# Performance work log

Measured on AMD Instinct MI355X. Metric: run time of the kernel, lower is better.

## Reference

```python
import jax, jax.numpy as jnp
import numpy as np

N_HEADS = 16
N_KV_HEADS = 4
HEAD_DIM = 128
D_MODEL = 2048
WINDOW = 1024
THETA = 10000.0
EPS = 1e-6


def _rmsnorm(x, w):
    var = jnp.mean(x * x, axis=-1, keepdims=True)
    return x * jax.lax.rsqrt(var + EPS) * w


def _rope(x, pos):
    # x: [B, H, S, D]; rotate-half (llama-style) RoPE
    d2 = HEAD_DIM // 2
    inv_freq = 1.0 / (THETA ** (jnp.arange(0, HEAD_DIM, 2, dtype=jnp.float32) / HEAD_DIM))
    ang = pos[:, None].astype(jnp.float32) * inv_freq[None, :]  # [S, D/2]
    cos = jnp.cos(ang)[None, None]
    sin = jnp.sin(ang)[None, None]
    x1, x2 = x[..., :d2], x[..., d2:]
    return jnp.concatenate([x1 * cos - x2 * sin, x1 * sin + x2 * cos], axis=-1)


def setup_inputs() -> dict:
    key = jax.random.key(0)
    ks = jax.random.split(key, 7)
    B, S = 1, 2048
    s = 0.02
    return {
        "x": jax.random.normal(ks[0], (B, S, D_MODEL), jnp.float32),
        "wq": jax.random.normal(ks[1], (N_HEADS * HEAD_DIM, D_MODEL), jnp.float32) * s,
        "wk": jax.random.normal(ks[2], (N_KV_HEADS * HEAD_DIM, D_MODEL), jnp.float32) * s,
        "wv": jax.random.normal(ks[3], (N_KV_HEADS * HEAD_DIM, D_MODEL), jnp.float32) * s,
        "wo": jax.random.normal(ks[4], (D_MODEL, N_HEADS * HEAD_DIM), jnp.float32) * s,
        "q_norm_w": jnp.ones((HEAD_DIM,), jnp.float32),
        "k_norm_w": jnp.ones((HEAD_DIM,), jnp.float32),
    }


def reference(x, wq, wk, wv, wo, q_norm_w, k_norm_w):
    B, S, _ = x.shape
    past_length = 0
    scale = HEAD_DIM ** -0.5
    n_rep = N_HEADS // N_KV_HEADS

    q = (x @ wq.T).reshape(B, S, N_HEADS, HEAD_DIM).transpose(0, 2, 1, 3)
    k = (x @ wk.T).reshape(B, S, N_KV_HEADS, HEAD_DIM).transpose(0, 2, 1, 3)
    v = (x @ wv.T).reshape(B, S, N_KV_HEADS, HEAD_DIM).transpose(0, 2, 1, 3)

    q = _rmsnorm(q, q_norm_w)
    k = _rmsnorm(k, k_norm_w)

    pos = jnp.arange(S) + past_length
    q = _rope(q, pos)
    k = _rope(k, pos)

    # GQA: materialize repeated KV heads, as in _repeat_kv
    k_rep = jnp.repeat(k, n_rep, axis=1)  # [B, H, S, D]
    v_rep = jnp.repeat(v, n_rep, axis=1)

    # sliding-window causal mask (total_seq_len=S > WINDOW)
    q_idx = jnp.arange(S)[:, None] + past_length
    k_idx = jnp.arange(S)[None, :]
    mask = (q_idx >= k_idx) & (q_idx - k_idx < WINDOW)  # [S, S]

    scores = jnp.einsum("bhqd,bhkd->bhqk", q, k_rep) * scale
    scores = jnp.where(mask[None, None], scores, jnp.float32(-jnp.inf))
    attn = jax.nn.softmax(scores, axis=-1)
    out = jnp.einsum("bhqk,bhkd->bhqd", attn, v_rep)

    out = out.transpose(0, 2, 1, 3).reshape(B, S, N_HEADS * HEAD_DIM)
    return out @ wo.T
```

## Files before the change

kernel.cpp:

```cpp
#include <hip/hip_runtime.h>
#include <hip/hip_bf16.h>
#include <cstdint>
#include <cstddef>

typedef __attribute__((ext_vector_type(4))) float f32x4;
typedef __attribute__((ext_vector_type(8))) short bf16x8;
typedef __attribute__((ext_vector_type(8))) unsigned short us8;

#define MFMA16(a, b, c) __builtin_amdgcn_mfma_f32_16x16x32_bf16(a, b, c, 0, 0, 0)

__device__ inline unsigned short f2bf(float f) {
    unsigned int u = __float_as_uint(f);
    u += 0x7fffu + ((u >> 16) & 1u);
    return (unsigned short)(u >> 16);
}
__device__ inline unsigned short f2bf_fast(float f) {
    float r;
    asm("v_cvt_pk_bf16_f32 %0, %1, %2" : "=v"(r) : "v"(f), "v"(f));
    return (unsigned short)__float_as_uint(r);
}

__device__ inline void gload_lds16(const void* g, void* l) {
    __builtin_amdgcn_global_load_lds(
        (const __attribute__((address_space(1))) void*)g,
        (__attribute__((address_space(3))) void*)l, 16, 0, 0);
}
__device__ inline unsigned lds_addr(const void* p) {
    return (unsigned)(size_t)((__attribute__((address_space(3))) const void*)p);
}

__global__ __launch_bounds__(256) void prep_all(const float* __restrict__ x,
                                                const float* __restrict__ wq,
                                                const float* __restrict__ wk,
                                                const float* __restrict__ wv,
                                                const float* __restrict__ wo,
                                                unsigned short* __restrict__ xb,
                                                unsigned short* __restrict__ wqkv,
                                                unsigned short* __restrict__ wob,
                                                float2* __restrict__ tbl) {
    const int b = blockIdx.x;
    if (b < 14336) {
        const float* src; unsigned short* dst; int off4;
        if (b < 4096)       { src = x;  dst = xb;                 off4 = b; }
        else if (b < 8192)  { src = wq; dst = wqkv;               off4 = b - 4096; }
        else if (b < 9216)  { src = wk; dst = wqkv + 2048 * 2048; off4 = b - 8192; }
        else if (b < 10240) { src = wv; dst = wqkv + 2560 * 2048; off4 = b - 9216; }
        else                { src = wo; dst = wob;                off4 = b - 10240; }
        int i = (off4 * 256 + threadIdx.x) * 4;
        float4 v = *(const float4*)(src + i);
        ushort4 o;
        o.x = f2bf(v.x); o.y = f2bf(v.y); o.z = f2bf(v.z); o.w = f2bf(v.w);
        *(ushort4*)(dst + i) = o;
    } else {
        int idx = (b - 14336) * 256 + threadIdx.x;
        int row = idx >> 6, t = idx & 63;
        float inv_freq = exp2f((float)t * (-2.0f / 128.0f) * 13.287712379549449f);
        float s, c;
        sincosf((float)row * inv_freq, &s, &c);
        tbl[idx] = make_float2(c, s);
    }
}

__global__ __launch_bounds__(512, 2) void gemm256(const unsigned short* __restrict__ A,
                                                  const unsigned short* __restrict__ B,
                                                  float* __restrict__ Cp,
                                                  int M, int N, int Kfull, int kspan) {
    __shared__ unsigned short As[3][8192];
    __shared__ unsigned short Bs[3][8192];
    const int tid = threadIdx.x;
    const int lane = tid & 63, wave = tid >> 6;
    const int wr = wave >> 2, wc = wave & 3;
    const int l15 = lane & 15, l4 = lane >> 4;
    const int gx = gridDim.x;
    const int nwg = gx * gridDim.y;
    const int bid0 = blockIdx.y * gx + blockIdx.x;
    const int q8 = nwg >> 3, r8 = nwg & 7;
    const int xcd = bid0 & 7, sub = bid0 >> 3;
    const int wgid = ((xcd < r8) ? xcd * (q8 + 1) : r8 * (q8 + 1) + (xcd - r8) * q8) + sub;
    const int bm = wgid / gx, bn = wgid % gx;
    const int z = blockIdx.z;
    const unsigned short* Az = A + (size_t)z * kspan;
    const unsigned short* Bz = B + (size_t)z * kspan;
    float* C = Cp + (size_t)z * M * N;
    const int nK = kspan >> 5;

    f32x4 acc[8][4] = {};

    const int r0 = tid >> 2, qs = tid & 3;
    const int qsw = qs ^ ((r0 >> 1) & 3);
    const unsigned short* pa0 = Az + (size_t)(bm * 256 + r0) * Kfull + qsw * 8;
    const unsigned short* pa1 = pa0 + (size_t)128 * Kfull;
    const unsigned short* pb0 = Bz + (size_t)(bn * 256 + r0) * Kfull + qsw * 8;
    const unsigned short* pb1 = pb0 + (size_t)128 * Kfull;

#define STG(kt, bb)                                            \
    do {                                                       \
        gload_lds16(pa0 + (kt) * 32, &As[bb][tid * 8]);        \
        gload_lds16(pa1 + (kt) * 32, &As[bb][4096 + tid * 8]); \
        gload_lds16(pb0 + (kt) * 32, &Bs[bb][tid * 8]);        \
        gload_lds16(pb1 + (kt) * 32, &Bs[bb][4096 + tid * 8]); \
    } while (0)

    const int q = l4 ^ ((l15 >> 1) & 3);
    const unsigned aB = lds_addr(&As[0][0]) + (unsigned)((wr * 128 + l15) * 64 + q * 16);
    const unsigned bB = lds_addr(&Bs[0][0]) + (unsigned)((wc * 64 + l15) * 64 + q * 16);

#define DSR(dst, addr, off) \
    asm volatile("ds_read_b128 %0, %1 offset:" #off : "=v"(dst) : "v"(addr))

    STG(0, 0);
    STG(1, 1);
    int bc = 0, bs = 2;
    for (int kt = 0; kt < nK; ++kt) {
        if (kt + 1 < nK)
            asm volatile("s_waitcnt vmcnt(4)\ns_barrier" ::: "memory");
        else
            asm volatile("s_waitcnt vmcnt(0)\ns_barrier" ::: "memory");
        __builtin_amdgcn_sched_barrier(0);

        bf16x8 a[8], b[4];
        {
            const unsigned aA = aB + bc * 16384;
            const unsigned bA = bB + bc * 16384;
            DSR(a[0], aA, 0);    DSR(a[1], aA, 1024);
            DSR(a[2], aA, 2048); DSR(a[3], aA, 3072);
            DSR(a[4], aA, 4096); DSR(a[5], aA, 5120);
            DSR(a[6], aA, 6144); DSR(a[7], aA, 7168);
            DSR(b[0], bA, 0);    DSR(b[1], bA, 1024);
            DSR(b[2], bA, 2048); DSR(b[3], bA, 3072);
        }
        if (kt + 2 < nK) STG(kt + 2, bs);
        asm volatile("s_waitcnt lgkmcnt(0)" ::: "memory");
        __builtin_amdgcn_sched_barrier(0);

        __builtin_amdgcn_s_setprio(1);
#pragma unroll
        for (int m = 0; m < 8; ++m)
#pragma unroll
            for (int n = 0; n < 4; ++n)
                acc[m][n] = MFMA16(a[m], b[n], acc[m][n]);
        __builtin_amdgcn_s_setprio(0);

        if (++bc == 3) bc = 0;
        if (++bs == 3) bs = 0;
    }
#undef STG
#undef DSR

    for (int m = 0; m < 8; ++m)
        for (int n = 0; n < 4; ++n)
            for (int j = 0; j < 4; ++j) {
                int row = bm * 256 + wr * 128 + m * 16 + l4 * 4 + j;
                int col = bn * 256 + wc * 64 + n * 16 + l15;
                C[(size_t)row * N + col] = acc[m][n][j];
            }
}

__global__ __launch_bounds__(256) void norm_rope(const float* __restrict__ p0,
                                                 const float* __restrict__ p1,
                                                 const float* __restrict__ qw,
                                                 const float* __restrict__ kw,
                                                 const float2* __restrict__ tbl,
                                                 unsigned short* __restrict__ Qb,
                                                 unsigned short* __restrict__ Kb) {
    const int row = blockIdx.x;
    const int head = blockIdx.y * 4 + (threadIdx.x >> 6);
    const int t = threadIdx.x & 63;
    const size_t off = (size_t)row * 3072 + head * 128;
    float x1 = p0[off + t] + p1[off + t];
    float x2 = p0[off + t + 64] + p1[off + t + 64];
    float ss = x1 * x1 + x2 * x2;
    for (int m = 32; m; m >>= 1) ss += __shfl_xor(ss, m);
    float r = rsqrtf(ss * (1.0f / 128.0f) + 1e-6f);
    const float* w = (head < 16) ? qw : kw;
    float y1 = x1 * r * w[t], y2 = x2 * r * w[t + 64];
    float2 cs = tbl[row * 64 + t];
    x1 = y1 * cs.x - y2 * cs.y;
    x2 = y1 * cs.y + y2 * cs.x;
    if (head < 16) {
        const float SCALE2 = 0.12751879526654698f;
        x1 *= SCALE2; x2 *= SCALE2;
    }
    unsigned short* dst = (head < 16) ? Qb + ((size_t)head * 2048 + row) * 128
                                      : Kb + ((size_t)(head - 16) * 2048 + row) * 128;
    dst[t] = f2bf(x1);
    dst[t + 64] = f2bf(x2);
}

__global__ __launch_bounds__(256) void transpose_v(const float* __restrict__ p0,
                                                   const float* __restrict__ p1,
                                                   unsigned short* __restrict__ VbT) {
    const int kt = blockIdx.x;
    const int h  = blockIdx.y;
    __shared__ unsigned short T[64 * 132];
    const int tid = threadIdx.x;
    for (int i = 0; i < 8; ++i) {
        int s = i * 256 + tid;
        int r = s >> 5, c = (s & 31) * 4;
        size_t off = (size_t)(kt * 64 + r) * 3072 + (20 + h) * 128 + c;
        float4 a = *(const float4*)(p0 + off);
        float4 b = *(const float4*)(p1 + off);
        ushort4 o;
        o.x = f2bf(a.x + b.x); o.y = f2bf(a.y + b.y);
        o.z = f2bf(a.z + b.z); o.w = f2bf(a.w + b.w);
        *(ushort4*)&T[r * 132 + c] = o;
    }
    __syncthreads();
    for (int i = 0; i < 4; ++i) {
        int s = i * 256 + tid;
        int d = s >> 3, ck = (s & 7) * 8;
        us8 v;
        for (int j = 0; j < 8; ++j) v[j] = T[(ck + j) * 132 + d];
        *(us8*)(VbT + (size_t)h * 128 * 2048 + (size_t)d * 2048 + kt * 64 + ck) = v;
    }
}

__global__ __launch_bounds__(256) void attn_fwd(const unsigned short* __restrict__ Qb,
                                                const unsigned short* __restrict__ Kb,
                                                const unsigned short* __restrict__ VbT,
                                                unsigned short* __restrict__ Ob) {
    const int bid = blockIdx.x;
    const int seq = bid >> 3;
    const int h = (bid & 7) * 2 + (seq >> 5);
    const int qt = seq & 31;
    const int kvh = h >> 2;
    const int q0 = qt * 64;
    __shared__ unsigned short Ks[2][64 * 128];
    __shared__ unsigned short Vs[2][128 * 64];
    __shared__ unsigned short Ps[4][16 * 72];
    const int tid = threadIdx.x;
    const int lane = tid & 63, wave = tid >> 6;
    const int l15 = lane & 15, l4 = lane >> 4;

    bf16x8 qf[4];
    {
        const unsigned short* qrow =
            Qb + ((size_t)h * 2048 + q0 + wave * 16 + l15) * 128 + l4 * 8;
        for (int kk = 0; kk < 4; ++kk) qf[kk] = *(const bf16x8*)(qrow + kk * 32);
    }
    f32x4 o[8] = {};
    float m2[4], lp[4];
    for (int j = 0; j < 4; ++j) { m2[j] = -1e30f; lp[j] = 0.0f; }
    const int kt_lo = (qt >= 16) ? (qt - 16) : 0;

    const unsigned short* Kh = Kb + (size_t)kvh * 2048 * 128;
    const unsigned short* Vh = VbT + (size_t)kvh * 128 * 2048;

    {
        const int kt = kt_lo;
        for (int i = 0; i < 4; ++i) {
            int s = i * 256 + tid;
            int r = s >> 4;
            int cb = ((s & 15) * 16) ^ ((r & 7) << 4);
            gload_lds16(Kh + (size_t)(kt * 64 + r) * 128 + (cb >> 1), &Ks[0][s * 8]);
        }
        for (int i = 0; i < 4; ++i) {
            int s = i * 256 + tid;
            int d = s >> 3;
            int cb = ((s & 7) * 16) ^ ((d & 7) << 4);
            gload_lds16(Vh + (size_t)d * 2048 + kt * 64 + (cb >> 1), &Vs[0][s * 8]);
        }
    }

    int cur = 0;
    for (int kt = kt_lo; kt <= qt; ++kt) {
        __syncthreads();

        if (kt < qt) {
            const int kn = kt + 1;
            for (int i = 0; i < 4; ++i) {
                int s = i * 256 + tid;
                int r = s >> 4;
                int cb = ((s & 15) * 16) ^ ((r & 7) << 4);
                gload_lds16(Kh + (size_t)(kn * 64 + r) * 128 + (cb >> 1), &Ks[cur ^ 1][s * 8]);
            }
            for (int i = 0; i < 4; ++i) {
                int s = i * 256 + tid;
                int d = s >> 3;
                int cb = ((s & 7) * 16) ^ ((d & 7) << 4);
                gload_lds16(Vh + (size_t)d * 2048 + kn * 64 + (cb >> 1), &Vs[cur ^ 1][s * 8]);
            }
        }

        f32x4 s[4] = {};
        __builtin_amdgcn_s_setprio(1);
        for (int nn = 0; nn < 4; ++nn)
            for (int kk = 0; kk < 4; ++kk) {
                int r = nn * 16 + l15;
                int cb = (kk * 64 + l4 * 16) ^ ((r & 7) << 4);
                bf16x8 kf = *(const bf16x8*)((const char*)&Ks[cur][0] + r * 256 + cb);
                s[nn] = MFMA16(qf[kk], kf, s[nn]);
            }
        __builtin_amdgcn_s_setprio(0);

        float p[4][4];
        const bool masked = (kt == qt) || (qt >= 16 && kt == kt_lo);
        if (masked) {
            for (int nn = 0; nn < 4; ++nn) {
                int kc = kt * 64 + nn * 16 + l15;
                for (int j = 0; j < 4; ++j) {
                    int qr = q0 + wave * 16 + l4 * 4 + j;
                    unsigned diff = (unsigned)(qr - kc);
                    p[nn][j] = (diff < 1024u) ? s[nn][j] : -1e30f;
                }
            }
        } else {
            for (int nn = 0; nn < 4; ++nn)
                for (int j = 0; j < 4; ++j) p[nn][j] = s[nn][j];
        }

        float mxl[4];
        bool flag = true;
        for (int j = 0; j < 4; ++j) {
            mxl[j] = fmaxf(fmaxf(p[0][j], p[1][j]), fmaxf(p[2][j], p[3][j]));
            flag = flag && (mxl[j] <= m2[j] + 11.0f);
        }
        if (!__all(flag)) {
            for (int j = 0; j < 4; ++j) {
                float mx = mxl[j];
                for (int mk = 8; mk; mk >>= 1) mx = fmaxf(mx, __shfl_xor(mx, mk));
                float mnew = fmaxf(m2[j], mx);
                float corr = exp2f(m2[j] - mnew);
                m2[j] = mnew;
                lp[j] *= corr;
                for (int dd = 0; dd < 8; ++dd) o[dd][j] *= corr;
            }
        }
        for (int j = 0; j < 4; ++j) {
            float rs = 0.0f;
            for (int nn = 0; nn < 4; ++nn) {
                float pv = exp2f(p[nn][j] - m2[j]);
                p[nn][j] = pv;
                rs += pv;
            }
            lp[j] += rs;
        }

        for (int j = 0; j < 4; ++j)
            for (int nn = 0; nn < 4; ++nn)
                Ps[wave][(l4 * 4 + j) * 72 + nn * 16 + l15] = f2bf_fast(p[nn][j]);

        bf16x8 pa[2];
        for (int kk2 = 0; kk2 < 2; ++kk2)
            pa[kk2] = *(const bf16x8*)&Ps[wave][l15 * 72 + kk2 * 32 + l4 * 8];

        __builtin_amdgcn_s_setprio(1);
        for (int dd = 0; dd < 8; ++dd)
            for (int kk2 = 0; kk2 < 2; ++kk2) {
                int d = dd * 16 + l15;
                int cb = (kk2 * 64 + l4 * 16) ^ ((d & 7) << 4);
                bf16x8 vf = *(const bf16x8*)((const char*)&Vs[cur][0] + d * 128 + cb);
                o[dd] = MFMA16(pa[kk2], vf, o[dd]);
            }
        __builtin_amdgcn_s_setprio(0);
        cur ^= 1;
    }

    for (int j = 0; j < 4; ++j) {
        float lt = lp[j];
        for (int mk = 8; mk; mk >>= 1) lt += __shfl_xor(lt, mk);
        float inv = 1.0f / lt;
        int row = q0 + wave * 16 + l4 * 4 + j;
        unsigned short* orow = Ob + (size_t)row * 2048 + h * 128;
        for (int dd = 0; dd < 8; ++dd) orow[dd * 16 + l15] = f2bf_fast(o[dd][j] * inv);
    }
}

__global__ __launch_bounds__(256) void add4(const float* __restrict__ p,
                                            float* __restrict__ out, int n) {
    int i = (blockIdx.x * 256 + threadIdx.x) * 4;
    if (i >= n) return;
    f32x4 a = *(const f32x4*)(p + i);
    f32x4 b = *(const f32x4*)(p + 4194304 + i);
    f32x4 c = *(const f32x4*)(p + 8388608 + i);
    f32x4 d = *(const f32x4*)(p + 12582912 + i);
    a = (a + b) + (c + d);
    *(f32x4*)(out + i) = a;
}

extern "C" void kernel_launch(void* const* d_in, const int* in_sizes, int n_in,
                              void* d_out, int out_size, void* d_ws, size_t ws_size,
                              hipStream_t stream) {
    const float* x  = (const float*)d_in[0];
    const float* wq = (const float*)d_in[1];
    const float* wk = (const float*)d_in[2];
    const float* wv = (const float*)d_in[3];
    const float* wo = (const float*)d_in[4];
    const float* qw = (const float*)d_in[5];
    const float* kw = (const float*)d_in[6];
    float* out = (float*)d_out;

    char* ws = (char*)d_ws;
    unsigned short* xb   = (unsigned short*)(ws + 0);
    unsigned short* wqkv = (unsigned short*)(ws + 8388608);
    unsigned short* wob  = (unsigned short*)(ws + 20971520);
    float*          qkvP = (float*)(ws + 29360128);
    unsigned short* Qb   = (unsigned short*)(ws + 79691776);
    unsigned short* Kb   = (unsigned short*)(ws + 88080384);
    unsigned short* VbT  = (unsigned short*)(ws + 92274688);
    float*          outP = (float*)(ws + 29360128);
    unsigned short* Ob   = (unsigned short*)(ws + 96468992);
    float2*         tbl  = (float2*)(ws + 104857600);

    prep_all<<<dim3(14848), dim3(256), 0, stream>>>(x, wq, wk, wv, wo, xb, wqkv, wob, tbl);
    gemm256<<<dim3(12, 8, 2), dim3(512), 0, stream>>>(xb, wqkv, qkvP, 2048, 3072, 2048, 1024);
    norm_rope<<<dim3(2048, 5), dim3(256), 0, stream>>>(qkvP, qkvP + 2048 * 3072, qw, kw, tbl, Qb, Kb);
    transpose_v<<<dim3(32, 4), dim3(256), 0, stream>>>(qkvP, qkvP + 2048 * 3072, VbT);
    attn_fwd<<<dim3(512), dim3(256), 0, stream>>>(Qb, Kb, VbT, Ob);
    gemm256<<<dim3(8, 8, 4), dim3(512), 0, stream>>>(Ob, wob, outP, 2048, 2048, 2048, 512);
    add4<<<dim3(4096), dim3(256), 0, stream>>>(outP, out, 2048 * 2048);
}
```

Baseline: 143.7 us.

## Store split-K GEMM partials as bf16 and single-buffer V in attention

```diff
diff --git a/kernel.cpp b/kernel.cpp
--- a/kernel.cpp
+++ b/kernel.cpp
@@ -13,6 +13,9 @@
     unsigned int u = __float_as_uint(f);
     u += 0x7fffu + ((u >> 16) & 1u);
     return (unsigned short)(u >> 16);
+}
+__device__ inline float bf2f(unsigned short u) {
+    return __uint_as_float((unsigned int)u << 16);
 }
 __device__ inline unsigned short f2bf_fast(float f) {
     float r;
@@ -63,7 +66,7 @@
 
 __global__ __launch_bounds__(512, 2) void gemm256(const unsigned short* __restrict__ A,
                                                   const unsigned short* __restrict__ B,
-                                                  float* __restrict__ Cp,
+                                                  unsigned short* __restrict__ Cp,
                                                   int M, int N, int Kfull, int kspan) {
     __shared__ unsigned short As[3][8192];
     __shared__ unsigned short Bs[3][8192];
@@ -81,7 +84,7 @@
     const int z = blockIdx.z;
     const unsigned short* Az = A + (size_t)z * kspan;
     const unsigned short* Bz = B + (size_t)z * kspan;
-    float* C = Cp + (size_t)z * M * N;
+    unsigned short* C = Cp + (size_t)z * M * N;
     const int nK = kspan >> 5;
 
     f32x4 acc[8][4] = {};
@@ -152,12 +155,12 @@
             for (int j = 0; j < 4; ++j) {
                 int row = bm * 256 + wr * 128 + m * 16 + l4 * 4 + j;
                 int col = bn * 256 + wc * 64 + n * 16 + l15;
-                C[(size_t)row * N + col] = acc[m][n][j];
-            }
-}
-
-__global__ __launch_bounds__(256) void norm_rope(const float* __restrict__ p0,
-                                                 const float* __restrict__ p1,
+                C[(size_t)row * N + col] = f2bf_fast(acc[m][n][j]);
+            }
+}
+
+__global__ __launch_bounds__(256) void norm_rope(const unsigned short* __restrict__ p0,
+                                                 const unsigned short* __restrict__ p1,
                                                  const float* __restrict__ qw,
                                                  const float* __restrict__ kw,
                                                  const float2* __restrict__ tbl,
@@ -167,8 +170,8 @@
     const int head = blockIdx.y * 4 + (threadIdx.x >> 6);
     const int t = threadIdx.x & 63;
     const size_t off = (size_t)row * 3072 + head * 128;
-    float x1 = p0[off + t] + p1[off + t];
-    float x2 = p0[off + t + 64] + p1[off + t + 64];
+    float x1 = bf2f(p0[off + t]) + bf2f(p1[off + t]);
+    float x2 = bf2f(p0[off + t + 64]) + bf2f(p1[off + t + 64]);
     float ss = x1 * x1 + x2 * x2;
     for (int m = 32; m; m >>= 1) ss += __shfl_xor(ss, m);
     float r = rsqrtf(ss * (1.0f / 128.0f) + 1e-6f);
@@ -187,8 +190,8 @@
     dst[t + 64] = f2bf(x2);
 }
 
-__global__ __launch_bounds__(256) void transpose_v(const float* __restrict__ p0,
-                                                   const float* __restrict__ p1,
+__global__ __launch_bounds__(256) void transpose_v(const unsigned short* __restrict__ p0,
+                                                   const unsigned short* __restrict__ p1,
                                                    unsigned short* __restrict__ VbT) {
     const int kt = blockIdx.x;
     const int h  = blockIdx.y;
@@ -198,11 +201,13 @@
         int s = i * 256 + tid;
         int r = s >> 5, c = (s & 31) * 4;
         size_t off = (size_t)(kt * 64 + r) * 3072 + (20 + h) * 128 + c;
-        float4 a = *(const float4*)(p0 + off);
-        float4 b = *(const float4*)(p1 + off);
+        ushort4 a = *(const ushort4*)(p0 + off);
+        ushort4 b = *(const ushort4*)(p1 + off);
         ushort4 o;
-        o.x = f2bf(a.x + b.x); o.y = f2bf(a.y + b.y);
-        o.z = f2bf(a.z + b.z); o.w = f2bf(a.w + b.w);
+        o.x = f2bf(bf2f(a.x) + bf2f(b.x));
+        o.y = f2bf(bf2f(a.y) + bf2f(b.y));
+        o.z = f2bf(bf2f(a.z) + bf2f(b.z));
+        o.w = f2bf(bf2f(a.w) + bf2f(b.w));
         *(ushort4*)&T[r * 132 + c] = o;
     }
     __syncthreads();
@@ -226,7 +231,7 @@
     const int kvh = h >> 2;
     const int q0 = qt * 64;
     __shared__ unsigned short Ks[2][64 * 128];
-    __shared__ unsigned short Vs[2][128 * 64];
+    __shared__ unsigned short Vs[128 * 64];
     __shared__ unsigned short Ps[4][16 * 72];
     const int tid = threadIdx.x;
     const int lane = tid & 63, wave = tid >> 6;
@@ -246,40 +251,29 @@
     const unsigned short* Kh = Kb + (size_t)kvh * 2048 * 128;
     const unsigned short* Vh = VbT + (size_t)kvh * 128 * 2048;
 
-    {
-        const int kt = kt_lo;
-        for (int i = 0; i < 4; ++i) {
-            int s = i * 256 + tid;
-            int r = s >> 4;
-            int cb = ((s & 15) * 16) ^ ((r & 7) << 4);
-            gload_lds16(Kh + (size_t)(kt * 64 + r) * 128 + (cb >> 1), &Ks[0][s * 8]);
-        }
-        for (int i = 0; i < 4; ++i) {
-            int s = i * 256 + tid;
-            int d = s >> 3;
-            int cb = ((s & 7) * 16) ^ ((d & 7) << 4);
-            gload_lds16(Vh + (size_t)d * 2048 + kt * 64 + (cb >> 1), &Vs[0][s * 8]);
-        }
-    }
+    int ksr[4], ksc[4], vsr[4], vsc[4];
+    for (int i = 0; i < 4; ++i) {
+        int s = i * 256 + tid;
+        ksr[i] = s >> 4;
+        ksc[i] = (((s & 15) * 16) ^ ((ksr[i] & 7) << 4)) >> 1;
+        vsr[i] = s >> 3;
+        vsc[i] = (((s & 7) * 16) ^ ((vsr[i] & 7) << 4)) >> 1;
+    }
+
+    for (int i = 0; i < 4; ++i)
+        gload_lds16(Kh + (size_t)(kt_lo * 64 + ksr[i]) * 128 + ksc[i], &Ks[0][(i * 256 + tid) * 8]);
 
     int cur = 0;
     for (int kt = kt_lo; kt <= qt; ++kt) {
-        __syncthreads();
-
+        asm volatile("s_waitcnt vmcnt(0)\ns_barrier" ::: "memory");
+        __builtin_amdgcn_sched_barrier(0);
+
+        for (int i = 0; i < 4; ++i)
+            gload_lds16(Vh + (size_t)vsr[i] * 2048 + kt * 64 + vsc[i], &Vs[(i * 256 + tid) * 8]);
         if (kt < qt) {
-            const int kn = kt + 1;
-            for (int i = 0; i < 4; ++i) {
-                int s = i * 256 + tid;
-                int r = s >> 4;
-                int cb = ((s & 15) * 16) ^ ((r & 7) << 4);
-                gload_lds16(Kh + (size_t)(kn * 64 + r) * 128 + (cb >> 1), &Ks[cur ^ 1][s * 8]);
-            }
-            for (int i = 0; i < 4; ++i) {
-                int s = i * 256 + tid;
-                int d = s >> 3;
-                int cb = ((s & 7) * 16) ^ ((d & 7) << 4);
-                gload_lds16(Vh + (size_t)d * 2048 + kn * 64 + (cb >> 1), &Vs[cur ^ 1][s * 8]);
-            }
+            for (int i = 0; i < 4; ++i)
+                gload_lds16(Kh + (size_t)((kt + 1) * 64 + ksr[i]) * 128 + ksc[i],
+                            &Ks[cur ^ 1][(i * 256 + tid) * 8]);
         }
 
         f32x4 s[4] = {};
@@ -344,12 +338,18 @@
         for (int kk2 = 0; kk2 < 2; ++kk2)
             pa[kk2] = *(const bf16x8*)&Ps[wave][l15 * 72 + kk2 * 32 + l4 * 8];
 
+        if (kt < qt)
+            asm volatile("s_waitcnt vmcnt(4)\ns_barrier" ::: "memory");
+        else
+            asm volatile("s_waitcnt vmcnt(0)\ns_barrier" ::: "memory");
+        __builtin_amdgcn_sched_barrier(0);
+
         __builtin_amdgcn_s_setprio(1);
         for (int dd = 0; dd < 8; ++dd)
             for (int kk2 = 0; kk2 < 2; ++kk2) {
                 int d = dd * 16 + l15;
                 int cb = (kk2 * 64 + l4 * 16) ^ ((d & 7) << 4);
-                bf16x8 vf = *(const bf16x8*)((const char*)&Vs[cur][0] + d * 128 + cb);
+                bf16x8 vf = *(const bf16x8*)((const char*)&Vs[0] + d * 128 + cb);
                 o[dd] = MFMA16(pa[kk2], vf, o[dd]);
             }
         __builtin_amdgcn_s_setprio(0);
@@ -366,16 +366,21 @@
     }
 }
 
-__global__ __launch_bounds__(256) void add4(const float* __restrict__ p,
+__global__ __launch_bounds__(256) void add4(const unsigned short* __restrict__ p,
                                             float* __restrict__ out, int n) {
-    int i = (blockIdx.x * 256 + threadIdx.x) * 4;
+    int i = (blockIdx.x * 256 + threadIdx.x) * 8;
     if (i >= n) return;
-    f32x4 a = *(const f32x4*)(p + i);
-    f32x4 b = *(const f32x4*)(p + 4194304 + i);
-    f32x4 c = *(const f32x4*)(p + 8388608 + i);
-    f32x4 d = *(const f32x4*)(p + 12582912 + i);
-    a = (a + b) + (c + d);
-    *(f32x4*)(out + i) = a;
+    us8 a = *(const us8*)(p + i);
+    us8 b = *(const us8*)(p + 4194304 + i);
+    us8 c = *(const us8*)(p + 8388608 + i);
+    us8 d = *(const us8*)(p + 12582912 + i);
+    f32x4 o0, o1;
+    for (int j = 0; j < 4; ++j)
+        o0[j] = (bf2f(a[j]) + bf2f(b[j])) + (bf2f(c[j]) + bf2f(d[j]));
+    for (int j = 0; j < 4; ++j)
+        o1[j] = (bf2f(a[j + 4]) + bf2f(b[j + 4])) + (bf2f(c[j + 4]) + bf2f(d[j + 4]));
+    *(f32x4*)(out + i) = o0;
+    *(f32x4*)(out + i + 4) = o1;
 }
 
 extern "C" void kernel_launch(void* const* d_in, const int* in_sizes, int n_in,
@@ -386,6 +391,7 @@
     const float* wk = (const float*)d_in[2];
     const float* wv = (const float*)d_in[3];
     const float* wo = (const float*)d_in[4];
+    const float* wo_ = wo; (void)wo_;
     const float* qw = (const float*)d_in[5];
     const float* kw = (const float*)d_in[6];
     float* out = (float*)d_out;
@@ -394,12 +400,12 @@
     unsigned short* xb   = (unsigned short*)(ws + 0);
     unsigned short* wqkv = (unsigned short*)(ws + 8388608);
     unsigned short* wob  = (unsigned short*)(ws + 20971520);
-    float*          qkvP = (float*)(ws + 29360128);
-    unsigned short* Qb   = (unsigned short*)(ws + 79691776);
-    unsigned short* Kb   = (unsigned short*)(ws + 88080384);
-    unsigned short* VbT  = (unsigned short*)(ws + 92274688);
-    float*          outP = (float*)(ws + 29360128);
-    unsigned short* Ob   = (unsigned short*)(ws + 96468992);
+    unsigned short* qkvP = (unsigned short*)(ws + 29360128);
+    unsigned short* Qb   = (unsigned short*)(ws + 54525952);
+    unsigned short* Kb   = (unsigned short*)(ws + 62914560);
+    unsigned short* VbT  = (unsigned short*)(ws + 65011712);
+    unsigned short* Ob   = (unsigned short*)(ws + 67108864);
+    unsigned short* outP = (unsigned short*)(ws + 29360128);
     float2*         tbl  = (float2*)(ws + 104857600);
 
     prep_all<<<dim3(14848), dim3(256), 0, stream>>>(x, wq, wk, wv, wo, xb, wqkv, wob, tbl);
@@ -408,5 +414,5 @@
     transpose_v<<<dim3(32, 4), dim3(256), 0, stream>>>(qkvP, qkvP + 2048 * 3072, VbT);
     attn_fwd<<<dim3(512), dim3(256), 0, stream>>>(Qb, Kb, VbT, Ob);
     gemm256<<<dim3(8, 8, 4), dim3(512), 0, stream>>>(Ob, wob, outP, 2048, 2048, 2048, 512);
-    add4<<<dim3(4096), dim3(256), 0, stream>>>(outP, out, 2048 * 2048);
-}
+    add4<<<dim3(2048), dim3(256), 0, stream>>>(outP, out, 2048 * 2048);
+}
```

New measurement: 133.7 us. 1.07x faster.
